# Performance work log

Measured on AMD Instinct MI355X. Metric: run time of the kernel, lower is better.

The kernel has to match this reference:

```python
import jax, jax.numpy as jnp
import numpy as np

N = 50000
D_IN = 128
HID = 128
HEADS = 4
PER_HEAD = HID // HEADS
NEG_SLOPE = 0.2


def gatv2_conv(x, src, dst, W_l, W_r, att, bias, H, C, n):
    """PyG GATv2Conv: x [n,F], src/dst [E] (self-loops already appended).
    out[i] = sum_{j->i} softmax_i(att . leaky_relu(Wl x_j + Wr x_i)) * (Wl x_j)
    """
    x_l = (x @ W_l).reshape(n, H, C)  # source-side transform
    x_r = (x @ W_r).reshape(n, H, C)  # destination-side transform
    e = jax.nn.leaky_relu(x_l[src] + x_r[dst], NEG_SLOPE)      # [E,H,C]
    alpha = jnp.einsum('ehc,hc->eh', e, att)                    # [E,H]
    # segment softmax over incoming edges of each destination node
    seg_max = jax.ops.segment_max(alpha, dst, num_segments=n)   # [n,H]
    alpha = jnp.exp(alpha - seg_max[dst])
    denom = jax.ops.segment_sum(alpha, dst, num_segments=n)     # [n,H]
    alpha = alpha / denom[dst]
    msg = x_l[src] * alpha[..., None]                           # [E,H,C]
    out = jax.ops.segment_sum(msg, dst, num_segments=n)         # [n,H,C]
    return out.reshape(n, H * C) + bias


def setup_inputs() -> dict:
    key = jax.random.key(0)
    ks = jax.random.split(key, 10)
    E = 800000
    x = jax.random.normal(ks[0], (N, D_IN), dtype=jnp.float32)
    edge_index = jax.random.randint(ks[1], (2, E), 0, N, dtype=jnp.int64)

    def glorot(k, shape):
        lim = float(np.sqrt(6.0 / (shape[0] + shape[1])))
        return jax.random.uniform(k, shape, jnp.float32, -lim, lim)

    # layer 1: GATv2Conv(D_IN, PER_HEAD, heads=HEADS, concat=True)
    W_l1 = glorot(ks[2], (D_IN, HEADS * PER_HEAD))
    W_r1 = glorot(ks[3], (D_IN, HEADS * PER_HEAD))
    att1 = glorot(ks[4], (HEADS, PER_HEAD))
    b1 = jnp.zeros((HEADS * PER_HEAD,), jnp.float32)
    # layer 2: GATv2Conv(HID, HID, heads=1, concat=True)
    W_l2 = glorot(ks[5], (HID, HID))
    W_r2 = glorot(ks[6], (HID, HID))
    att2 = glorot(ks[7], (1, HID))
    b2 = jnp.zeros((HID,), jnp.float32)
    return {"x": x, "edge_index": edge_index,
            "W_l1": W_l1, "W_r1": W_r1, "att1": att1, "b1": b1,
            "W_l2": W_l2, "W_r2": W_r2, "att2": att2, "b2": b2}


def reference(x, edge_index, W_l1, W_r1, att1, b1, W_l2, W_r2, att2, b2):
    # add self-loops (PyG GATv2Conv default add_self_loops=True)
    loops = jnp.arange(N, dtype=edge_index.dtype)
    src = jnp.concatenate([edge_index[0], loops])
    dst = jnp.concatenate([edge_index[1], loops])
    h = gatv2_conv(x, src, dst, W_l1, W_r1, att1, b1, HEADS, PER_HEAD, N)
    h = jax.nn.relu(h)
    out = gatv2_conv(h, src, dst, W_l2, W_r2, att2, b2, 1, HID, N)
    return out
```

## Files before the change

### kernel.cpp

```cpp
#include <hip/hip_runtime.h>
#include <hip/hip_fp16.h>
#include <math.h>


#define NEG_SLOPE 0.2f
#define CHUNKS 128
#define DCAP 8192

typedef _Float16 half8 __attribute__((ext_vector_type(8)));
typedef _Float16 half4 __attribute__((ext_vector_type(4)));
typedef _Float16 half2v __attribute__((ext_vector_type(2)));
typedef float floatx4 __attribute__((ext_vector_type(4)));

#if defined(__has_builtin)
#if __has_builtin(__builtin_amdgcn_fdot2)
#define HAVE_FDOT2 1
#endif
#endif

template <int CTRL>
__device__ __forceinline__ float dppmov(float x) {
    int xi = __builtin_bit_cast(int, x);
    int r  = __builtin_amdgcn_update_dpp(0, xi, CTRL, 0xF, 0xF, true);
    return __builtin_bit_cast(float, r);
}
#define DPP_XOR1  0xB1
#define DPP_XOR2  0x4E
#define DPP_HMIRR 0x141
#define DPP_MIRR  0x140


__device__ __forceinline__ void sortA_body(int c, const int* __restrict__ dstA,
                                           int* __restrict__ hist_mat,
                                           int E, int Et, int csz) {
    __shared__ int hist[256];
    int tid = threadIdx.x;
    hist[tid] = 0;
    __syncthreads();
    int start = c * csz, stop = min(Et, start + csz);
    for (int e = start + tid; e < stop; e += 256) {
        int d = (e < E) ? dstA[e] : (e - E);
        atomicAdd(&hist[d >> 8], 1);
    }
    __syncthreads();
    hist_mat[c * 256 + tid] = hist[tid];
}

__device__ __forceinline__ void convert_body(int t,
        const float* __restrict__ Wl1, const float* __restrict__ Wr1,
        const float* __restrict__ Wl2, const float* __restrict__ Wr2,
        const float* __restrict__ att1, const float* __restrict__ att2,
        _Float16* __restrict__ Wt1, _Float16* __restrict__ Wt2,
        _Float16* __restrict__ attH) {
    if (t < 65536) {
        int layer = t >> 15;
        int id = t & 32767;
        int c = id >> 7, k = id & 127;
        const float* Wl = layer ? Wl2 : Wl1;
        const float* Wr = layer ? Wr2 : Wr1;
        _Float16* Wt = layer ? Wt2 : Wt1;
        float v = (c < 128) ? Wl[(size_t)k * 128 + c] : Wr[(size_t)k * 128 + (c - 128)];
        Wt[(size_t)c * 128 + k] = (_Float16)v;
    } else {
        int id = t - 65536;
        if (id < 256) {
            float v = (id < 128) ? att1[id] : att2[id - 128];
            attH[id] = (_Float16)v;
        }
    }
}

__device__ __forceinline__ void sortC_body(int c, const int* __restrict__ srcA,
        const int* __restrict__ dstA, const int* __restrict__ offs_flat,
        int* __restrict__ packed, int E, int Et, int csz) {
    __shared__ int pos[256];
    int tid = threadIdx.x;
    pos[tid] = offs_flat[tid * CHUNKS + c];
    __syncthreads();
    int start = c * csz, stop = min(Et, start + csz);
    for (int e = start + tid; e < stop; e += 256) {
        int s, d;
        if (e < E) { s = srcA[e]; d = dstA[e]; } else { s = e - E; d = s; }
        int p = atomicAdd(&pos[d >> 8], 1);
        packed[p] = ((d & 255) << 16) | s;
    }
}

#define BPAD 136

template <bool AF32>
__device__ __forceinline__ void gemm_body(int bid, const void* __restrict__ Av,
        const _Float16* __restrict__ Bt, _Float16* __restrict__ outL,
        _Float16* __restrict__ outR, int n) {
    __shared__ _Float16 sB[256 * BPAD];
    int tid = threadIdx.x;
    {
        int c0 = (tid & 15) * 8;
        int r0 = tid >> 4;
        #pragma unroll
        for (int i = 0; i < 16; ++i) {
            int r = r0 + i * 16;
            *(half8*)(sB + r * BPAD + c0) = *(const half8*)(Bt + (size_t)r * 128 + c0);
        }
    }
    int wave = tid >> 6;
    int lane = tid & 63;
    int ln = lane & 15;
    int q  = lane >> 4;
    int row0 = bid * 64 + wave * 16;

    int arow = row0 + ln;
    if (arow >= n) arow = n - 1;
    half8 a0, a1, a2, a3;
    if (AF32) {
        const float* ap = (const float*)Av + (size_t)arow * 128 + q * 8;
        #pragma unroll
        for (int g = 0; g < 4; ++g) {
            float4 f0 = *(const float4*)(ap + g * 32);
            float4 f1 = *(const float4*)(ap + g * 32 + 4);
            half8 h;
            h[0] = (_Float16)f0.x; h[1] = (_Float16)f0.y;
            h[2] = (_Float16)f0.z; h[3] = (_Float16)f0.w;
            h[4] = (_Float16)f1.x; h[5] = (_Float16)f1.y;
            h[6] = (_Float16)f1.z; h[7] = (_Float16)f1.w;
            if (g == 0) a0 = h; else if (g == 1) a1 = h;
            else if (g == 2) a2 = h; else a3 = h;
        }
    } else {
        const _Float16* ap = (const _Float16*)Av + (size_t)arow * 128 + q * 8;
        a0 = *(const half8*)(ap);
        a1 = *(const half8*)(ap + 32);
        a2 = *(const half8*)(ap + 64);
        a3 = *(const half8*)(ap + 96);
    }

    __syncthreads();

    floatx4 acc[16];
    #pragma unroll
    for (int ct = 0; ct < 16; ++ct) {
        const _Float16* bp = sB + (ct * 16 + ln) * BPAD + q * 8;
        half8 b0 = *(const half8*)(bp);
        half8 b1 = *(const half8*)(bp + 32);
        half8 b2 = *(const half8*)(bp + 64);
        half8 b3 = *(const half8*)(bp + 96);
        floatx4 c = {0.f, 0.f, 0.f, 0.f};
        c = __builtin_amdgcn_mfma_f32_16x16x32_f16(b0, a0, c, 0, 0, 0);
        c = __builtin_amdgcn_mfma_f32_16x16x32_f16(b1, a1, c, 0, 0, 0);
        c = __builtin_amdgcn_mfma_f32_16x16x32_f16(b2, a2, c, 0, 0, 0);
        c = __builtin_amdgcn_mfma_f32_16x16x32_f16(b3, a3, c, 0, 0, 0);
        acc[ct] = c;
    }

    int grow = row0 + ln;
    if (grow < n) {
        #pragma unroll
        for (int ct = 0; ct < 16; ++ct) {
            int colb = ct * 16 + q * 4;
            half4 hv;
            hv[0] = (_Float16)acc[ct][0];
            hv[1] = (_Float16)acc[ct][1];
            hv[2] = (_Float16)acc[ct][2];
            hv[3] = (_Float16)acc[ct][3];
            _Float16* dst = (ct < 8) ? (outL + (size_t)grow * 128 + colb)
                                     : (outR + (size_t)grow * 128 + (colb - 128));
            *(half4*)dst = hv;
        }
    }
}


__global__ __launch_bounds__(256)
void fused_pre(const int* __restrict__ dstA, int* __restrict__ hist_mat,
               int E, int Et, int csz,
               const float* __restrict__ Wl1, const float* __restrict__ Wr1,
               const float* __restrict__ Wl2, const float* __restrict__ Wr2,
               const float* __restrict__ att1, const float* __restrict__ att2,
               _Float16* __restrict__ Wt1, _Float16* __restrict__ Wt2,
               _Float16* __restrict__ attH) {
    if (blockIdx.x < CHUNKS) {
        sortA_body(blockIdx.x, dstA, hist_mat, E, Et, csz);
    } else {
        int t = (blockIdx.x - CHUNKS) * 256 + threadIdx.x;
        convert_body(t, Wl1, Wr1, Wl2, Wr2, att1, att2, Wt1, Wt2, attH);
    }
}

__global__ __launch_bounds__(1024)
void sortB_scan(const int* __restrict__ hist_mat, int* __restrict__ offs_flat) {
    __shared__ int wsum[16];
    int t = threadIdx.x;
    int lane = t & 63, wid = t >> 6;
    int carry = 0;
    for (int it = 0; it < 8; ++it) {
        int f0 = it * 4096 + t * 4;
        int v[4];
        #pragma unroll
        for (int k = 0; k < 4; ++k) {
            int f = f0 + k;
            v[k] = hist_mat[(f & 127) * 256 + (f >> 7)];
        }
        int s1 = v[0] + v[1], s2 = s1 + v[2], s3 = s2 + v[3];
        int x = s3;
        #pragma unroll
        for (int off = 1; off < 64; off <<= 1) {
            int y = __shfl_up(x, off, 64);
            if (lane >= off) x += y;
        }
        if (lane == 63) wsum[wid] = x;
        __syncthreads();
        if (wid == 0) {
            int s = (lane < 16) ? wsum[lane] : 0;
            #pragma unroll
            for (int off = 1; off < 16; off <<= 1) {
                int y = __shfl_up(s, off, 64);
                if (lane >= off) s += y;
            }
            if (lane < 16) wsum[lane] = s;
        }
        __syncthreads();
        int woff = (wid == 0) ? 0 : wsum[wid - 1];
        int excl = carry + woff + x - s3;
        offs_flat[f0 + 0] = excl;
        offs_flat[f0 + 1] = excl + v[0];
        offs_flat[f0 + 2] = excl + s1;
        offs_flat[f0 + 3] = excl + s2;
        carry += wsum[15];
        __syncthreads();
    }
}

__global__ __launch_bounds__(256)
void fused_mid(const int* __restrict__ srcA, const int* __restrict__ dstA,
               const int* __restrict__ offs_flat, int* __restrict__ packed,
               int E, int Et, int csz,
               const float* __restrict__ X, const _Float16* __restrict__ Wt1,
               _Float16* __restrict__ outL, _Float16* __restrict__ outR, int n) {
    if (blockIdx.x < CHUNKS) {
        sortC_body(blockIdx.x, srcA, dstA, offs_flat, packed, E, Et, csz);
    } else {
        gemm_body<true>(blockIdx.x - CHUNKS, X, Wt1, outL, outR, n);
    }
}

__global__ __launch_bounds__(256)
void gemm_l2(const _Float16* __restrict__ A, const _Float16* __restrict__ Bt,
             _Float16* __restrict__ outL, _Float16* __restrict__ outR, int n) {
    gemm_body<false>(blockIdx.x, A, Bt, outL, outR, n);
}

__global__ __launch_bounds__(256)
void sortD_fine(const int* __restrict__ offs_flat, const int* __restrict__ packed,
                int* __restrict__ rowptr, int* __restrict__ srcs,
                int n, int Et, int nbuck) {
    __shared__ int stage[DCAP];
    __shared__ int sorted[DCAP];
    __shared__ int hist[256], curv[256], wsumD[4];
    int tid = threadIdx.x, b = blockIdx.x;
    int base = offs_flat[b * CHUNKS];
    int end  = (b == nbuck - 1) ? Et : offs_flat[(b + 1) * CHUNKS];
    int m = min(end - base, DCAP);

    hist[tid] = 0;
    for (int i = tid; i < m; i += 256) stage[i] = packed[base + i];
    __syncthreads();
    for (int i = tid; i < m; i += 256) atomicAdd(&hist[stage[i] >> 16], 1);
    __syncthreads();
    {
        int v = hist[tid];
        int lane = tid & 63, w = tid >> 6;
        int x = v;
        #pragma unroll
        for (int off = 1; off < 64; off <<= 1) {
            int y = __shfl_up(x, off, 64);
            if (lane >= off) x += y;
        }
        if (lane == 63) wsumD[w] = x;
        __syncthreads();
        int woff = 0;
        for (int i = 0; i < w; ++i) woff += wsumD[i];
        int excl = woff + x - v;
        curv[tid] = excl;
        int node0 = b << 8;
        if (node0 + tid < n) rowptr[node0 + tid] = base + excl;
        if (b == 0 && tid == 0) rowptr[n] = Et;
    }
    __syncthreads();
    for (int i = tid; i < m; i += 256) {
        int p = stage[i];
        int pos = atomicAdd(&curv[p >> 16], 1);
        sorted[pos] = p & 0xFFFF;
    }
    __syncthreads();
    for (int i = tid; i < m; i += 256) srcs[base + i] = sorted[i];
}


template <bool LAYER1>
__global__ __launch_bounds__(256)
void edge_aggregate(const _Float16* __restrict__ xl, const _Float16* __restrict__ xr,
                    const _Float16* __restrict__ attH, const float* __restrict__ bias,
                    const int* __restrict__ rowptr, const int* __restrict__ srcs,
                    void* __restrict__ outv, int n) {
    int node = blockIdx.x * (blockDim.x >> 6) + (threadIdx.x >> 6);
    int lane = threadIdx.x & 63;
    if (node >= n) return;
    int ln = lane & 15;
    int q  = lane >> 4;
    int c0 = ln * 8;

    half8 xrh = *(const half8*)(xr + (size_t)node * 128 + c0);
    half8 ahh = *(const half8*)(attH + c0);

    float acc[8] = {0.f, 0.f, 0.f, 0.f, 0.f, 0.f, 0.f, 0.f};
    float l = 0.f;

    auto proc = [&](half8 vh, bool valid) {
        half8 e  = vh + xrh;
        half8 es = e * (_Float16)NEG_SLOPE;
        half8 lr = __builtin_elementwise_max(e, es);
        float p = 0.f;
        #pragma unroll
        for (int k = 0; k < 4; ++k) {
            half2v ee = { lr[2 * k], lr[2 * k + 1] };
            half2v aa = { ahh[2 * k], ahh[2 * k + 1] };
#ifdef HAVE_FDOT2
            p = __builtin_amdgcn_fdot2(ee, aa, p, false);
#else
            p = fmaf((float)ee[0], (float)aa[0], p);
            p = fmaf((float)ee[1], (float)aa[1], p);
#endif
        }
        p += dppmov<DPP_XOR1>(p);
        p += dppmov<DPP_XOR2>(p);
        if (!LAYER1) { p += dppmov<DPP_HMIRR>(p); p += dppmov<DPP_MIRR>(p); }
        float pe = __expf(p);
        if (!valid) pe = 0.f;
        l += pe;
        #pragma unroll
        for (int k = 0; k < 8; ++k) acc[k] = fmaf(pe, (float)vh[k], acc[k]);
    };

    int jb = rowptr[node], je = rowptr[node + 1];
    for (int base = jb; base < je; base += 64) {
        int idx = base + lane;
        int myS = (idx < je) ? srcs[idx] : 0;
        int cnt = min(64, je - base);
        int t = 0;
        for (; t + 16 <= cnt; t += 16) {
            int s0 = __shfl(myS, t + q, 64);
            int s1 = __shfl(myS, t + 4 + q, 64);
            int s2 = __shfl(myS, t + 8 + q, 64);
            int s3 = __shfl(myS, t + 12 + q, 64);
            half8 v0 = *(const half8*)(xl + (size_t)s0 * 128 + c0);
            half8 v1 = *(const half8*)(xl + (size_t)s1 * 128 + c0);
            half8 v2 = *(const half8*)(xl + (size_t)s2 * 128 + c0);
            half8 v3 = *(const half8*)(xl + (size_t)s3 * 128 + c0);
            proc(v0, true); proc(v1, true); proc(v2, true); proc(v3, true);
        }
        for (; t < cnt; t += 4) {
            int sa = __shfl(myS, t + q, 64);
            half8 va = *(const half8*)(xl + (size_t)sa * 128 + c0);
            proc(va, (t + q) < cnt);
        }
    }

    #pragma unroll
    for (int k = 0; k < 8; ++k) {
        acc[k] += __shfl_xor(acc[k], 16, 64);
        acc[k] += __shfl_xor(acc[k], 32, 64);
    }
    l += __shfl_xor(l, 16, 64);
    l += __shfl_xor(l, 32, 64);

    float inv = 1.0f / l;
    float bv[8];
    *(float4*)&bv[0] = *(const float4*)(bias + c0);
    *(float4*)&bv[4] = *(const float4*)(bias + c0 + 4);
    float o[8];
    #pragma unroll
    for (int k = 0; k < 8; ++k) {
        o[k] = acc[k] * inv + bv[k];
        if (LAYER1) o[k] = fmaxf(o[k], 0.f);
    }
    if (lane < 16) {
        if (LAYER1) {
            __half2 hh2[4];
            #pragma unroll
            for (int k = 0; k < 4; ++k) hh2[k] = __floats2half2_rn(o[2 * k], o[2 * k + 1]);
            *(float4*)((_Float16*)outv + (size_t)node * 128 + c0) = *(float4*)&hh2[0];
        } else {
            float* out = (float*)outv;
            *(float4*)(out + (size_t)node * 128 + c0)     = *(float4*)&o[0];
            *(float4*)(out + (size_t)node * 128 + c0 + 4) = *(float4*)&o[4];
        }
    }
}


extern "C" void kernel_launch(void* const* d_in, const int* in_sizes, int n_in,
                              void* d_out, int out_size, void* d_ws, size_t ws_size,
                              hipStream_t stream) {
    const float* x    = (const float*)d_in[0];
    const int*   ei   = (const int*)d_in[1];
    const float* Wl1  = (const float*)d_in[2];
    const float* Wr1  = (const float*)d_in[3];
    const float* att1 = (const float*)d_in[4];
    const float* b1   = (const float*)d_in[5];
    const float* Wl2  = (const float*)d_in[6];
    const float* Wr2  = (const float*)d_in[7];
    const float* att2 = (const float*)d_in[8];
    const float* b2   = (const float*)d_in[9];

    int n  = in_sizes[0] / 128;
    int E  = in_sizes[1] / 2;
    int Et = E + n;

    _Float16* xlh  = (_Float16*)d_ws;
    _Float16* xrh2 = xlh + (size_t)n * 128;
    _Float16* hh   = xrh2 + (size_t)n * 128;
    _Float16* Wt1  = hh  + (size_t)n * 128;
    _Float16* Wt2  = Wt1 + 256 * 128;
    _Float16* attH = Wt2 + 256 * 128;
    int* rowptr   = (int*)(attH + 256);
    int* srcs     = rowptr + (n + 1);
    int* packed   = srcs + Et;
    int* hist_mat = packed + Et;
    int* offs_flat= hist_mat + CHUNKS * 256;

    const int* srcA = ei;
    const int* dstA = ei + E;

    int csz   = (Et + CHUNKS - 1) / CHUNKS;
    int nbuck = (n + 255) >> 8;
    int gemm_grid = (n + 63) / 64;
    int edge_grid = (n + 3) / 4;

    fused_pre<<<CHUNKS + 257, 256, 0, stream>>>(
        dstA, hist_mat, E, Et, csz,
        Wl1, Wr1, Wl2, Wr2, att1, att2, Wt1, Wt2, attH);
    sortB_scan<<<1, 1024, 0, stream>>>(hist_mat, offs_flat);
    fused_mid<<<CHUNKS + gemm_grid, 256, 0, stream>>>(
        srcA, dstA, offs_flat, packed, E, Et, csz,
        x, Wt1, xlh, xrh2, n);
    sortD_fine<<<nbuck, 256, 0, stream>>>(offs_flat, packed, rowptr, srcs, n, Et, nbuck);
    edge_aggregate<true><<<edge_grid, 256, 0, stream>>>(
        xlh, xrh2, attH, b1, rowptr, srcs, hh, n);
    gemm_l2<<<gemm_grid, 256, 0, stream>>>(hh, Wt2, xlh, xrh2, n);
    edge_aggregate<false><<<edge_grid, 256, 0, stream>>>(
        xlh, xrh2, attH + 128, b2, rowptr, srcs, d_out, n);
}
```

Measured before the change: 225.7 us.

## Split edge aggregation by channel slice per block; two-pass layer-2 attention

Edge kernels now give each block one 32-channel slice (a head in layer 1) of 32 nodes, with 16 lanes per node, so consecutive blocks touch the same slice of gathered rows and the cache working set shrinks. Layer 2 is split into two kernels: one computes partial attention logits per slice into a workspace buffer, and a second sums the four partials, applies exp and aggregates. This adds a global round trip of the logits and an extra launch, and the srcs/rowptr reads are repeated across the eight slice blocks.

```diff
diff --git a/kernel.cpp b/kernel.cpp
--- a/kernel.cpp
+++ b/kernel.cpp
@@ -26,8 +26,8 @@
 }
 #define DPP_XOR1  0xB1
 #define DPP_XOR2  0x4E
-#define DPP_HMIRR 0x141
-#define DPP_MIRR  0x140
+#define DPP_ROR4  0x124
+#define DPP_ROR8  0x128
 
 
 __device__ __forceinline__ void sortA_body(int c, const int* __restrict__ dstA,
@@ -296,21 +296,26 @@
 }
 
 
-template <bool LAYER1>
-__global__ __launch_bounds__(256)
-void edge_aggregate(const _Float16* __restrict__ xl, const _Float16* __restrict__ xr,
-                    const _Float16* __restrict__ attH, const float* __restrict__ bias,
-                    const int* __restrict__ rowptr, const int* __restrict__ srcs,
-                    void* __restrict__ outv, int n) {
-    int node = blockIdx.x * (blockDim.x >> 6) + (threadIdx.x >> 6);
-    int lane = threadIdx.x & 63;
+__global__ __launch_bounds__(256)
+void edge_l1(const _Float16* __restrict__ xl, const _Float16* __restrict__ xr,
+             const _Float16* __restrict__ attH, const float* __restrict__ bias,
+             const int* __restrict__ rowptr, const int* __restrict__ srcs,
+             _Float16* __restrict__ out, int n) {
+    int b = blockIdx.x;
+    int q8 = b & 7;
+    int h  = q8 >> 1;
+    int hs = q8 & 1;
+    int tid = threadIdx.x;
+    int grp = tid >> 4;
+    int l16 = tid & 15;
+    int quad = l16 >> 2;
+    int lq   = l16 & 3;
+    int node = (b >> 3) * 32 + hs * 16 + grp;
     if (node >= n) return;
-    int ln = lane & 15;
-    int q  = lane >> 4;
-    int c0 = ln * 8;
-
-    half8 xrh = *(const half8*)(xr + (size_t)node * 128 + c0);
-    half8 ahh = *(const half8*)(attH + c0);
+    int cb = h * 32 + lq * 8;
+
+    half8 xrh = *(const half8*)(xr + (size_t)node * 128 + cb);
+    half8 ahh = *(const half8*)(attH + cb);
 
     float acc[8] = {0.f, 0.f, 0.f, 0.f, 0.f, 0.f, 0.f, 0.f};
     float l = 0.f;
@@ -333,7 +338,6 @@
         }
         p += dppmov<DPP_XOR1>(p);
         p += dppmov<DPP_XOR2>(p);
-        if (!LAYER1) { p += dppmov<DPP_HMIRR>(p); p += dppmov<DPP_MIRR>(p); }
         float pe = __expf(p);
         if (!valid) pe = 0.f;
         l += pe;
@@ -342,58 +346,177 @@
     };
 
     int jb = rowptr[node], je = rowptr[node + 1];
-    for (int base = jb; base < je; base += 64) {
-        int idx = base + lane;
-        int myS = (idx < je) ? srcs[idx] : 0;
-        int cnt = min(64, je - base);
-        int t = 0;
-        for (; t + 16 <= cnt; t += 16) {
-            int s0 = __shfl(myS, t + q, 64);
-            int s1 = __shfl(myS, t + 4 + q, 64);
-            int s2 = __shfl(myS, t + 8 + q, 64);
-            int s3 = __shfl(myS, t + 12 + q, 64);
-            half8 v0 = *(const half8*)(xl + (size_t)s0 * 128 + c0);
-            half8 v1 = *(const half8*)(xl + (size_t)s1 * 128 + c0);
-            half8 v2 = *(const half8*)(xl + (size_t)s2 * 128 + c0);
-            half8 v3 = *(const half8*)(xl + (size_t)s3 * 128 + c0);
-            proc(v0, true); proc(v1, true); proc(v2, true); proc(v3, true);
-        }
-        for (; t < cnt; t += 4) {
-            int sa = __shfl(myS, t + q, 64);
-            half8 va = *(const half8*)(xl + (size_t)sa * 128 + c0);
-            proc(va, (t + q) < cnt);
-        }
+    int t = jb;
+    for (; t + 8 <= je; t += 8) {
+        int s0 = srcs[t + quad];
+        int s1 = srcs[t + 4 + quad];
+        half8 v0 = *(const half8*)(xl + (size_t)s0 * 128 + cb);
+        half8 v1 = *(const half8*)(xl + (size_t)s1 * 128 + cb);
+        proc(v0, true);
+        proc(v1, true);
+    }
+    for (; t < je; t += 4) {
+        int idx = t + quad;
+        int s = srcs[min(idx, je - 1)];
+        half8 v = *(const half8*)(xl + (size_t)s * 128 + cb);
+        proc(v, idx < je);
     }
 
     #pragma unroll
     for (int k = 0; k < 8; ++k) {
-        acc[k] += __shfl_xor(acc[k], 16, 64);
-        acc[k] += __shfl_xor(acc[k], 32, 64);
-    }
-    l += __shfl_xor(l, 16, 64);
-    l += __shfl_xor(l, 32, 64);
-
-    float inv = 1.0f / l;
-    float bv[8];
-    *(float4*)&bv[0] = *(const float4*)(bias + c0);
-    *(float4*)&bv[4] = *(const float4*)(bias + c0 + 4);
-    float o[8];
+        acc[k] += dppmov<DPP_ROR4>(acc[k]);
+        acc[k] += dppmov<DPP_ROR8>(acc[k]);
+    }
+    l += dppmov<DPP_ROR4>(l);
+    l += dppmov<DPP_ROR8>(l);
+
+    if (quad == 0) {
+        float inv = 1.0f / l;
+        float bv[8];
+        *(float4*)&bv[0] = *(const float4*)(bias + cb);
+        *(float4*)&bv[4] = *(const float4*)(bias + cb + 4);
+        __half2 hh2[4];
+        #pragma unroll
+        for (int k = 0; k < 4; ++k) {
+            float o0 = fmaxf(acc[2 * k] * inv + bv[2 * k], 0.f);
+            float o1 = fmaxf(acc[2 * k + 1] * inv + bv[2 * k + 1], 0.f);
+            hh2[k] = __floats2half2_rn(o0, o1);
+        }
+        *(float4*)(out + (size_t)node * 128 + cb) = *(float4*)&hh2[0];
+    }
+}
+
+__global__ __launch_bounds__(256)
+void e1_l2(const _Float16* __restrict__ xl, const _Float16* __restrict__ xr,
+           const _Float16* __restrict__ attH2,
+           const int* __restrict__ rowptr, const int* __restrict__ srcs,
+           float* __restrict__ pbuf, int n, int Et) {
+    int b = blockIdx.x;
+    int q8 = b & 7;
+    int sl = q8 >> 1;
+    int hs = q8 & 1;
+    int tid = threadIdx.x;
+    int grp = tid >> 4;
+    int l16 = tid & 15;
+    int quad = l16 >> 2;
+    int lq   = l16 & 3;
+    int node = (b >> 3) * 32 + hs * 16 + grp;
+    if (node >= n) return;
+    int cb = sl * 32 + lq * 8;
+
+    half8 xrh = *(const half8*)(xr + (size_t)node * 128 + cb);
+    half8 ahh = *(const half8*)(attH2 + cb);
+    float* pout = pbuf + (size_t)sl * Et;
+
+    auto pdot = [&](half8 vh) -> float {
+        half8 e  = vh + xrh;
+        half8 es = e * (_Float16)NEG_SLOPE;
+        half8 lr = __builtin_elementwise_max(e, es);
+        float p = 0.f;
+        #pragma unroll
+        for (int k = 0; k < 4; ++k) {
+            half2v ee = { lr[2 * k], lr[2 * k + 1] };
+            half2v aa = { ahh[2 * k], ahh[2 * k + 1] };
+#ifdef HAVE_FDOT2
+            p = __builtin_amdgcn_fdot2(ee, aa, p, false);
+#else
+            p = fmaf((float)ee[0], (float)aa[0], p);
+            p = fmaf((float)ee[1], (float)aa[1], p);
+#endif
+        }
+        p += dppmov<DPP_XOR1>(p);
+        p += dppmov<DPP_XOR2>(p);
+        return p;
+    };
+
+    int jb = rowptr[node], je = rowptr[node + 1];
+    int t = jb;
+    for (; t + 8 <= je; t += 8) {
+        int i0 = t + quad, i1 = t + 4 + quad;
+        int s0 = srcs[i0];
+        int s1 = srcs[i1];
+        half8 v0 = *(const half8*)(xl + (size_t)s0 * 128 + cb);
+        half8 v1 = *(const half8*)(xl + (size_t)s1 * 128 + cb);
+        float p0 = pdot(v0);
+        float p1 = pdot(v1);
+        if (lq == 0) { pout[i0] = p0; pout[i1] = p1; }
+    }
+    for (; t < je; t += 4) {
+        int idx = t + quad;
+        int s = srcs[min(idx, je - 1)];
+        half8 v = *(const half8*)(xl + (size_t)s * 128 + cb);
+        float p = pdot(v);
+        if (lq == 0 && idx < je) pout[idx] = p;
+    }
+}
+
+__global__ __launch_bounds__(256)
+void e2_l2(const _Float16* __restrict__ xl, const float* __restrict__ pbuf,
+           const float* __restrict__ bias,
+           const int* __restrict__ rowptr, const int* __restrict__ srcs,
+           float* __restrict__ out, int n, int Et) {
+    int b = blockIdx.x;
+    int q8 = b & 7;
+    int sl = q8 >> 1;
+    int hs = q8 & 1;
+    int tid = threadIdx.x;
+    int grp = tid >> 4;
+    int l16 = tid & 15;
+    int quad = l16 >> 2;
+    int lq   = l16 & 3;
+    int node = (b >> 3) * 32 + hs * 16 + grp;
+    if (node >= n) return;
+    int cb = sl * 32 + lq * 8;
+
+    float acc[8] = {0.f, 0.f, 0.f, 0.f, 0.f, 0.f, 0.f, 0.f};
+    float l = 0.f;
+
+    auto proc = [&](half8 vh, int idx, bool valid) {
+        float p = pbuf[idx] + pbuf[Et + idx] + pbuf[2 * (size_t)Et + idx]
+                + pbuf[3 * (size_t)Et + idx];
+        float pe = __expf(p);
+        if (!valid) pe = 0.f;
+        l += pe;
+        #pragma unroll
+        for (int k = 0; k < 8; ++k) acc[k] = fmaf(pe, (float)vh[k], acc[k]);
+    };
+
+    int jb = rowptr[node], je = rowptr[node + 1];
+    int t = jb;
+    for (; t + 8 <= je; t += 8) {
+        int i0 = t + quad, i1 = t + 4 + quad;
+        int s0 = srcs[i0];
+        int s1 = srcs[i1];
+        half8 v0 = *(const half8*)(xl + (size_t)s0 * 128 + cb);
+        half8 v1 = *(const half8*)(xl + (size_t)s1 * 128 + cb);
+        proc(v0, i0, true);
+        proc(v1, i1, true);
+    }
+    for (; t < je; t += 4) {
+        int idx = t + quad;
+        int ic = min(idx, je - 1);
+        int s = srcs[ic];
+        half8 v = *(const half8*)(xl + (size_t)s * 128 + cb);
+        proc(v, ic, idx < je);
+    }
+
     #pragma unroll
     for (int k = 0; k < 8; ++k) {
-        o[k] = acc[k] * inv + bv[k];
-        if (LAYER1) o[k] = fmaxf(o[k], 0.f);
-    }
-    if (lane < 16) {
-        if (LAYER1) {
-            __half2 hh2[4];
-            #pragma unroll
-            for (int k = 0; k < 4; ++k) hh2[k] = __floats2half2_rn(o[2 * k], o[2 * k + 1]);
-            *(float4*)((_Float16*)outv + (size_t)node * 128 + c0) = *(float4*)&hh2[0];
-        } else {
-            float* out = (float*)outv;
-            *(float4*)(out + (size_t)node * 128 + c0)     = *(float4*)&o[0];
-            *(float4*)(out + (size_t)node * 128 + c0 + 4) = *(float4*)&o[4];
-        }
+        acc[k] += dppmov<DPP_ROR4>(acc[k]);
+        acc[k] += dppmov<DPP_ROR8>(acc[k]);
+    }
+    l += dppmov<DPP_ROR4>(l);
+    l += dppmov<DPP_ROR8>(l);
+
+    if (quad == 0) {
+        float inv = 1.0f / l;
+        float bv[8], o[8];
+        *(float4*)&bv[0] = *(const float4*)(bias + cb);
+        *(float4*)&bv[4] = *(const float4*)(bias + cb + 4);
+        #pragma unroll
+        for (int k = 0; k < 8; ++k) o[k] = acc[k] * inv + bv[k];
+        *(float4*)(out + (size_t)node * 128 + cb)     = *(float4*)&o[0];
+        *(float4*)(out + (size_t)node * 128 + cb + 4) = *(float4*)&o[4];
     }
 }
 
@@ -427,6 +550,7 @@
     int* packed   = srcs + Et;
     int* hist_mat = packed + Et;
     int* offs_flat= hist_mat + CHUNKS * 256;
+    float* pbuf   = (float*)(offs_flat + CHUNKS * 256);
 
     const int* srcA = ei;
     const int* dstA = ei + E;
@@ -434,7 +558,7 @@
     int csz   = (Et + CHUNKS - 1) / CHUNKS;
     int nbuck = (n + 255) >> 8;
     int gemm_grid = (n + 63) / 64;
-    int edge_grid = (n + 3) / 4;
+    int sgrid = 8 * ((n + 31) / 32);
 
     fused_pre<<<CHUNKS + 257, 256, 0, stream>>>(
         dstA, hist_mat, E, Et, csz,
@@ -444,9 +568,8 @@
         srcA, dstA, offs_flat, packed, E, Et, csz,
         x, Wt1, xlh, xrh2, n);
     sortD_fine<<<nbuck, 256, 0, stream>>>(offs_flat, packed, rowptr, srcs, n, Et, nbuck);
-    edge_aggregate<true><<<edge_grid, 256, 0, stream>>>(
-        xlh, xrh2, attH, b1, rowptr, srcs, hh, n);
+    edge_l1<<<sgrid, 256, 0, stream>>>(xlh, xrh2, attH, b1, rowptr, srcs, hh, n);
     gemm_l2<<<gemm_grid, 256, 0, stream>>>(hh, Wt2, xlh, xrh2, n);
-    edge_aggregate<false><<<edge_grid, 256, 0, stream>>>(
-        xlh, xrh2, attH + 128, b2, rowptr, srcs, d_out, n);
-}
+    e1_l2<<<sgrid, 256, 0, stream>>>(xlh, xrh2, attH + 128, rowptr, srcs, pbuf, n, Et);
+    e2_l2<<<sgrid, 256, 0, stream>>>(xlh, pbuf, b2, rowptr, srcs, (float*)d_out, n, Et);
+}
```

Measured after the change: 300.4 us. 1.33x slower.
